# Kernel tuning notes

Hardware: AMD Instinct MI355X
Metric: run time of the kernel (lower is better)

The kernel has to match this reference:

```python
import jax, jax.numpy as jnp
import numpy as np


def setup_inputs() -> dict:
    key = jax.random.key(0)
    ks = jax.random.split(key, 6)
    B, O, L, D, D2 = 32, 1, 2048, 1024, 512
    query = jax.random.normal(ks[0], (B, O, D), dtype=jnp.float32)
    context = jax.random.normal(ks[1], (B, L, D), dtype=jnp.float32)
    W_in = jax.random.normal(ks[2], (D, D), dtype=jnp.float32) * (1.0 / np.sqrt(D))
    W_out = jax.random.normal(ks[3], (D2, 2 * D), dtype=jnp.float32) * (1.0 / np.sqrt(2 * D))
    ae = jax.random.uniform(ks[4], (B, 1, 1), dtype=jnp.float32)
    ab = jax.random.uniform(ks[5], (B, 1, 1), dtype=jnp.float32)
    return {"query": query, "context": context, "W_in": W_in, "W_out": W_out, "ae": ae, "ab": ab}


def reference(query, context, W_in, W_out, ae, ab):
    B, O, D = query.shape  # O == 1 (required by the broadcast in mix)
    L = context.shape[1]
    # linear_in (no bias): q @ W_in^T
    q = jnp.einsum('bod,ed->boe', query, W_in)  # [B,1,D]
    # attention scores + softmax over key dimension
    scores = jnp.einsum('bod,bld->bol', q, context)  # [B,1,L]
    attn = jax.nn.softmax(scores, axis=-1)  # [B,1,L]
    # mix: weights broadcast against context^T -> [B,D,L]
    mix = attn * jnp.transpose(context, (0, 2, 1))
    # temporal decay bias: delta_t = [L-1, ..., 0]
    delta_t = jnp.arange(L - 1, -1, -1, dtype=jnp.float32).reshape(1, 1, L)
    bt = jnp.exp(-ab * delta_t)  # [B,1,L]
    term_2 = jax.nn.relu(ae * mix * bt)  # [B,D,L]
    mixed = jnp.sum(term_2 + mix, axis=-1)[:, None, :]  # [B,1,D]
    combined = jnp.concatenate([mixed, q], axis=2)  # [B,1,2D]
    out = jnp.tanh(jnp.einsum('boc,ec->boe', combined, W_out))  # [B,1,D2]
    return (out, attn)
```

## Files before the change

kernel.cpp:

```cpp
#include <hip/hip_runtime.h>
#include <hip/hip_bf16.h>
#include <math.h>

#define NB 32
#define NL 2048
#define ND 1024
#define ND2 512
#define CH 32
#define ROWS (NL / CH)
#define RPW (ROWS / 4)

__device__ __forceinline__ float waveReduceSumAll(float v) {
    for (int off = 32; off > 0; off >>= 1) v += __shfl_xor(v, off, 64);
    return v;
}
__device__ __forceinline__ float waveReduceSum(float v) {
    for (int off = 32; off > 0; off >>= 1) v += __shfl_down(v, off, 64);
    return v;
}

__global__ __launch_bounds__(256) void k_qproj(const float* __restrict__ query,
                                               const float* __restrict__ W_in,
                                               float* __restrict__ q) {
    int wave = blockIdx.x * 4 + (threadIdx.x >> 6);
    int lane = threadIdx.x & 63;
    int b = wave >> 10;
    int e = wave & 1023;
    const float4* qr = (const float4*)(query + (size_t)b * ND) + lane * 4;
    const float4* wr = (const float4*)(W_in + (size_t)e * ND) + lane * 4;
    float s = 0.f;
#pragma unroll
    for (int t = 0; t < 4; t++) {
        float4 a = qr[t], w = wr[t];
        s += a.x * w.x + a.y * w.y + a.z * w.z + a.w * w.w;
    }
    s = waveReduceSum(s);
    if (lane == 0) q[b * ND + e] = s;
}

__global__ __launch_bounds__(256) void k_flash(const float* __restrict__ q,
                                               const float* __restrict__ ctx,
                                               const float* __restrict__ ae,
                                               const float* __restrict__ ab,
                                               float* __restrict__ scores,
                                               float* __restrict__ pm,
                                               float* __restrict__ pZ,
                                               float* __restrict__ pacc) {
    int b = blockIdx.x >> 5;
    int chunk = blockIdx.x & 31;
    int wave = threadIdx.x >> 6;
    int lane = threadIdx.x & 63;

    const float4* qp = (const float4*)(q + (size_t)b * ND) + lane * 4;
    float4 q0 = qp[0], q1 = qp[1], q2 = qp[2], q3 = qp[3];
    float aev = ae[b], abv = ab[b];

    float m = -INFINITY, Z = 0.f;
    float acc[16];
#pragma unroll
    for (int j = 0; j < 16; j++) acc[j] = 0.f;

    int l0 = chunk * ROWS + wave * RPW;
    for (int i = 0; i < RPW; i++) {
        int l = l0 + i;
        const float4* cp = (const float4*)(ctx + ((size_t)b * NL + l) * ND) + lane * 4;
        float4 c0 = cp[0], c1 = cp[1], c2 = cp[2], c3 = cp[3];
        float s = c0.x*q0.x + c0.y*q0.y + c0.z*q0.z + c0.w*q0.w
                + c1.x*q1.x + c1.y*q1.y + c1.z*q1.z + c1.w*q1.w
                + c2.x*q2.x + c2.y*q2.y + c2.z*q2.z + c2.w*q2.w
                + c3.x*q3.x + c3.y*q3.y + c3.z*q3.z + c3.w*q3.w;
        s = waveReduceSumAll(s);
        if (lane == 0) scores[b * NL + l] = s;

        float bt = __expf(-abv * (float)(NL - 1 - l));
        if (s > m) {
            float sc = __expf(m - s);
            m = s;
            Z *= sc;
#pragma unroll
            for (int j = 0; j < 16; j++) acc[j] *= sc;
        }
        float p = __expf(s - m);
        float k2 = p * aev * bt;
        Z += p;
        float c[16] = {c0.x,c0.y,c0.z,c0.w, c1.x,c1.y,c1.z,c1.w,
                       c2.x,c2.y,c2.z,c2.w, c3.x,c3.y,c3.z,c3.w};
#pragma unroll
        for (int j = 0; j < 16; j++)
            acc[j] += p * c[j] + k2 * fmaxf(c[j], 0.f);
    }

    __shared__ float sacc[4 * ND];
    __shared__ float sm[4], sZ[4];
#pragma unroll
    for (int j = 0; j < 16; j++) sacc[wave * ND + lane * 16 + j] = acc[j];
    if (lane == 0) { sm[wave] = m; sZ[wave] = Z; }
    __syncthreads();

    int tid = threadIdx.x;
    float m0 = sm[0], m1 = sm[1], m2 = sm[2], m3 = sm[3];
    float mb = fmaxf(fmaxf(m0, m1), fmaxf(m2, m3));
    float e0 = __expf(m0 - mb), e1 = __expf(m1 - mb),
          e2 = __expf(m2 - mb), e3 = __expf(m3 - mb);
    int d = tid * 4;
    float4 v;
    v.x = e0*sacc[0*ND+d+0] + e1*sacc[1*ND+d+0] + e2*sacc[2*ND+d+0] + e3*sacc[3*ND+d+0];
    v.y = e0*sacc[0*ND+d+1] + e1*sacc[1*ND+d+1] + e2*sacc[2*ND+d+1] + e3*sacc[3*ND+d+1];
    v.z = e0*sacc[0*ND+d+2] + e1*sacc[1*ND+d+2] + e2*sacc[2*ND+d+2] + e3*sacc[3*ND+d+2];
    v.w = e0*sacc[0*ND+d+3] + e1*sacc[1*ND+d+3] + e2*sacc[2*ND+d+3] + e3*sacc[3*ND+d+3];
    *(float4*)(pacc + ((size_t)(b * CH + chunk)) * ND + d) = v;
    if (tid == 0) {
        pm[b * CH + chunk] = mb;
        pZ[b * CH + chunk] = e0*sZ[0] + e1*sZ[1] + e2*sZ[2] + e3*sZ[3];
    }
}

__global__ __launch_bounds__(256) void k_merge(const float* __restrict__ pm,
                                               const float* __restrict__ pZ,
                                               const float* __restrict__ pacc,
                                               const float* __restrict__ scores,
                                               float* __restrict__ mixed,
                                               float* __restrict__ attn_out) {
    int b = blockIdx.x;
    int tid = threadIdx.x;
    __shared__ float ew[CH];
    __shared__ float smg, sinvZ;
    if (tid == 0) {
        float mg = -INFINITY;
        for (int i = 0; i < CH; i++) mg = fmaxf(mg, pm[b * CH + i]);
        float Zg = 0.f;
        for (int i = 0; i < CH; i++) Zg += __expf(pm[b * CH + i] - mg) * pZ[b * CH + i];
        smg = mg; sinvZ = 1.f / Zg;
    }
    __syncthreads();
    float mg = smg, invZ = sinvZ;
    if (tid < CH) ew[tid] = __expf(pm[b * CH + tid] - mg);
    __syncthreads();

    int d = tid * 4;
    float4 accv = {0.f, 0.f, 0.f, 0.f};
    for (int i = 0; i < CH; i++) {
        float4 pv = *(const float4*)(pacc + ((size_t)(b * CH + i)) * ND + d);
        float e = ew[i];
        accv.x += e * pv.x; accv.y += e * pv.y;
        accv.z += e * pv.z; accv.w += e * pv.w;
    }
    accv.x *= invZ; accv.y *= invZ; accv.z *= invZ; accv.w *= invZ;
    *(float4*)(mixed + (size_t)b * ND + d) = accv;

    for (int l = tid; l < NL; l += 256)
        attn_out[b * NL + l] = __expf(scores[b * NL + l] - mg) * invZ;
}

__global__ __launch_bounds__(256) void k_out(const float* __restrict__ mixed,
                                             const float* __restrict__ q,
                                             const float* __restrict__ W_out,
                                             float* __restrict__ out) {
    int wave = blockIdx.x * 4 + (threadIdx.x >> 6);
    int lane = threadIdx.x & 63;
    int b = wave >> 9;
    int e = wave & 511;
    int c0 = lane * 32;
    const float* src = (lane < 32) ? (mixed + (size_t)b * ND + c0)
                                   : (q + (size_t)b * ND + c0 - ND);
    const float4* wr = (const float4*)(W_out + (size_t)e * 2 * ND + c0);
    const float4* sp = (const float4*)src;
    float s = 0.f;
#pragma unroll
    for (int t = 0; t < 8; t++) {
        float4 w = wr[t], x = sp[t];
        s += w.x * x.x + w.y * x.y + w.z * x.z + w.w * x.w;
    }
    s = waveReduceSum(s);
    if (lane == 0) out[b * ND2 + e] = tanhf(s);
}

extern "C" void kernel_launch(void* const* d_in, const int* in_sizes, int n_in,
                              void* d_out, int out_size, void* d_ws, size_t ws_size,
                              hipStream_t stream) {
    const float* query = (const float*)d_in[0];
    const float* ctx   = (const float*)d_in[1];
    const float* W_in  = (const float*)d_in[2];
    const float* W_out = (const float*)d_in[3];
    const float* ae    = (const float*)d_in[4];
    const float* ab    = (const float*)d_in[5];
    float* out = (float*)d_out;
    float* attn_out = out + (size_t)NB * ND2;

    float* ws     = (float*)d_ws;
    float* q      = ws;
    float* scores = ws + 32768;
    float* pm     = ws + 98304;
    float* pZ     = ws + 99328;
    float* pacc   = ws + 100352;
    float* mixed  = ws + 1148928;

    k_qproj<<<8192, 256, 0, stream>>>(query, W_in, q);
    k_flash<<<NB * CH, 256, 0, stream>>>(q, ctx, ae, ab, scores, pm, pZ, pacc);
    k_merge<<<NB, 256, 0, stream>>>(pm, pZ, pacc, scores, mixed, attn_out);
    k_out<<<4096, 256, 0, stream>>>(mixed, q, W_out, out);
}
```

Before: 429.7 us.

## Batch four context rows per iteration with lazy softmax rescale and split merge kernel

The flash kernel now loads four context rows at once and interleaves their wave reductions, which raises memory-level parallelism and amortizes the shuffle latency. Max rescaling is applied only when the block max exceeds the running max by more than 8, which cuts down on rescale branches. The merge kernel is split across eight blocks per batch so more CUs share the reduction and the attn write. In exchange, register pressure rises, and the lazy rescale allows p values up to e^8, which stays safe in fp32.

After: 427.8 us. Within noise of the previous version (-0.5%).

```diff
diff --git a/kernel.cpp b/kernel.cpp
--- a/kernel.cpp
+++ b/kernel.cpp
@@ -9,11 +9,8 @@
 #define CH 32
 #define ROWS (NL / CH)
 #define RPW (ROWS / 4)
-
-__device__ __forceinline__ float waveReduceSumAll(float v) {
-    for (int off = 32; off > 0; off >>= 1) v += __shfl_xor(v, off, 64);
-    return v;
-}
+#define MSPLIT 8
+
 __device__ __forceinline__ float waveReduceSum(float v) {
     for (int off = 32; off > 0; off >>= 1) v += __shfl_down(v, off, 64);
     return v;
@@ -61,33 +58,52 @@
     for (int j = 0; j < 16; j++) acc[j] = 0.f;
 
     int l0 = chunk * ROWS + wave * RPW;
-    for (int i = 0; i < RPW; i++) {
-        int l = l0 + i;
-        const float4* cp = (const float4*)(ctx + ((size_t)b * NL + l) * ND) + lane * 4;
-        float4 c0 = cp[0], c1 = cp[1], c2 = cp[2], c3 = cp[3];
-        float s = c0.x*q0.x + c0.y*q0.y + c0.z*q0.z + c0.w*q0.w
-                + c1.x*q1.x + c1.y*q1.y + c1.z*q1.z + c1.w*q1.w
-                + c2.x*q2.x + c2.y*q2.y + c2.z*q2.z + c2.w*q2.w
-                + c3.x*q3.x + c3.y*q3.y + c3.z*q3.z + c3.w*q3.w;
-        s = waveReduceSumAll(s);
-        if (lane == 0) scores[b * NL + l] = s;
-
-        float bt = __expf(-abv * (float)(NL - 1 - l));
-        if (s > m) {
-            float sc = __expf(m - s);
-            m = s;
+    for (int i = 0; i < RPW; i += 4) {
+        const float* rowb = ctx + ((size_t)b * NL + (l0 + i)) * ND;
+        float4 c[4][4];
+        float s[4];
+#pragma unroll
+        for (int r = 0; r < 4; r++) {
+            const float4* cp = (const float4*)(rowb + (size_t)r * ND) + lane * 4;
+            c[r][0] = cp[0]; c[r][1] = cp[1]; c[r][2] = cp[2]; c[r][3] = cp[3];
+            s[r] = c[r][0].x*q0.x + c[r][0].y*q0.y + c[r][0].z*q0.z + c[r][0].w*q0.w
+                 + c[r][1].x*q1.x + c[r][1].y*q1.y + c[r][1].z*q1.z + c[r][1].w*q1.w
+                 + c[r][2].x*q2.x + c[r][2].y*q2.y + c[r][2].z*q2.z + c[r][2].w*q2.w
+                 + c[r][3].x*q3.x + c[r][3].y*q3.y + c[r][3].z*q3.z + c[r][3].w*q3.w;
+        }
+#pragma unroll
+        for (int off = 32; off > 0; off >>= 1) {
+#pragma unroll
+            for (int r = 0; r < 4; r++) s[r] += __shfl_xor(s[r], off, 64);
+        }
+        if (lane == 0)
+            *(float4*)(scores + (size_t)b * NL + l0 + i) =
+                make_float4(s[0], s[1], s[2], s[3]);
+
+        float bmax = fmaxf(fmaxf(s[0], s[1]), fmaxf(s[2], s[3]));
+        if (bmax > m + 8.f) {
+            float sc = __expf(m - bmax);
+            m = bmax;
             Z *= sc;
 #pragma unroll
             for (int j = 0; j < 16; j++) acc[j] *= sc;
         }
-        float p = __expf(s - m);
-        float k2 = p * aev * bt;
-        Z += p;
-        float c[16] = {c0.x,c0.y,c0.z,c0.w, c1.x,c1.y,c1.z,c1.w,
-                       c2.x,c2.y,c2.z,c2.w, c3.x,c3.y,c3.z,c3.w};
-#pragma unroll
-        for (int j = 0; j < 16; j++)
-            acc[j] += p * c[j] + k2 * fmaxf(c[j], 0.f);
+#pragma unroll
+        for (int r = 0; r < 4; r++) {
+            int l = l0 + i + r;
+            float bt = __expf(-abv * (float)(NL - 1 - l));
+            float p = __expf(s[r] - m);
+            float k2 = p * aev * bt;
+            Z += p;
+#pragma unroll
+            for (int t = 0; t < 4; t++) {
+                float4 cv = c[r][t];
+                acc[t * 4 + 0] += p * cv.x + k2 * fmaxf(cv.x, 0.f);
+                acc[t * 4 + 1] += p * cv.y + k2 * fmaxf(cv.y, 0.f);
+                acc[t * 4 + 2] += p * cv.z + k2 * fmaxf(cv.z, 0.f);
+                acc[t * 4 + 3] += p * cv.w + k2 * fmaxf(cv.w, 0.f);
+            }
+        }
     }
 
     __shared__ float sacc[4 * ND];
@@ -121,7 +137,8 @@
                                                const float* __restrict__ scores,
                                                float* __restrict__ mixed,
                                                float* __restrict__ attn_out) {
-    int b = blockIdx.x;
+    int b = blockIdx.x >> 3;
+    int slice = blockIdx.x & 7;
     int tid = threadIdx.x;
     __shared__ float ew[CH];
     __shared__ float smg, sinvZ;
@@ -134,22 +151,23 @@
     }
     __syncthreads();
     float mg = smg, invZ = sinvZ;
-    if (tid < CH) ew[tid] = __expf(pm[b * CH + tid] - mg);
+    if (tid < CH) ew[tid] = __expf(pm[b * CH + tid] - mg) * invZ;
     __syncthreads();
 
-    int d = tid * 4;
-    float4 accv = {0.f, 0.f, 0.f, 0.f};
-    for (int i = 0; i < CH; i++) {
-        float4 pv = *(const float4*)(pacc + ((size_t)(b * CH + i)) * ND + d);
-        float e = ew[i];
-        accv.x += e * pv.x; accv.y += e * pv.y;
-        accv.z += e * pv.z; accv.w += e * pv.w;
-    }
-    accv.x *= invZ; accv.y *= invZ; accv.z *= invZ; accv.w *= invZ;
-    *(float4*)(mixed + (size_t)b * ND + d) = accv;
-
-    for (int l = tid; l < NL; l += 256)
-        attn_out[b * NL + l] = __expf(scores[b * NL + l] - mg) * invZ;
+    if (tid < 32) {
+        int d = slice * (ND / MSPLIT) + tid * 4;
+        float4 accv = {0.f, 0.f, 0.f, 0.f};
+        for (int i = 0; i < CH; i++) {
+            float4 pv = *(const float4*)(pacc + ((size_t)(b * CH + i)) * ND + d);
+            float e = ew[i];
+            accv.x += e * pv.x; accv.y += e * pv.y;
+            accv.z += e * pv.z; accv.w += e * pv.w;
+        }
+        *(float4*)(mixed + (size_t)b * ND + d) = accv;
+    }
+
+    int l = slice * (NL / MSPLIT) + tid;
+    attn_out[b * NL + l] = __expf(scores[b * NL + l] - mg) * invZ;
 }
 
 __global__ __launch_bounds__(256) void k_out(const float* __restrict__ mixed,
@@ -197,6 +215,6 @@
 
     k_qproj<<<8192, 256, 0, stream>>>(query, W_in, q);
     k_flash<<<NB * CH, 256, 0, stream>>>(q, ctx, ae, ab, scores, pm, pZ, pacc);
-    k_merge<<<NB, 256, 0, stream>>>(pm, pZ, pacc, scores, mixed, attn_out);
+    k_merge<<<NB * MSPLIT, 256, 0, stream>>>(pm, pZ, pacc, scores, mixed, attn_out);
     k_out<<<4096, 256, 0, stream>>>(mixed, q, W_out, out);
 }
```
